# Kernel tuning notes

Measured on AMD Instinct MI355X. Metric: run time of the kernel, lower is better.

The kernel has to match this reference:

```python
import jax, jax.numpy as jnp
import numpy as np

# Straight-through hard softmax (gumbel_softmax with use_gumbel=False, hard=True, dim=1)
def _st_softmax(logits, axis=1):
    soft = jax.nn.softmax(logits, axis=axis)
    hard = jax.nn.one_hot(jnp.argmax(soft, axis=axis), logits.shape[axis], axis=axis, dtype=soft.dtype)
    return soft + jax.lax.stop_gradient(hard - soft)

# gumbel_sigmoid with k=2, hard=True, use_gumbel=False: two straight-through
# one-hot masks selecting the top-1 and top-2 entries along dim=1.
def _st_top2(logits):  # logits: [1, D, S] -> two masks [1, D, S]
    soft = jax.nn.softmax(logits, axis=1)
    D = logits.shape[1]
    _, idx = jax.lax.top_k(jnp.swapaxes(soft, 1, 2), 2)  # [1, S, 2]
    h1 = jnp.swapaxes(jax.nn.one_hot(idx[..., 0], D, dtype=soft.dtype), 1, 2)
    h2 = jnp.swapaxes(jax.nn.one_hot(idx[..., 1], D, dtype=soft.dtype), 1, 2)
    return (soft + jax.lax.stop_gradient(h1 - soft),
            soft + jax.lax.stop_gradient(h2 - soft))

B, CIN, HW, M_IMG, S0 = 8192, 8, 28, 8, 4
S1, S2, M_SC = 3, 2, 2
F_IN, H_IMG, O_IMG = 784, 256, 3  # img_module_arch
H_SC = 12                          # module_arch [2,12,1]

def setup_inputs() -> dict:
    key = jax.random.key(0)
    ks = jax.random.split(key, 16)
    def w(k, shape, fan_in):
        return jax.random.normal(k, shape, jnp.float32) / np.sqrt(fan_in)
    d = {}
    d['x'] = jax.random.normal(ks[0], (B, CIN, HW, HW), jnp.float32)
    # routing embeddings (torch.randn init)
    d['inp_emb0'] = jax.random.normal(ks[1], (1, CIN, S0), jnp.float32)
    d['loc_emb0'] = jax.random.normal(ks[2], (1, M_IMG, S0), jnp.float32)
    d['inp_emb1'] = jax.random.normal(ks[3], (1, S0 * O_IMG, S1), jnp.float32)
    d['loc_emb1'] = jax.random.normal(ks[4], (1, M_SC, S1), jnp.float32)
    d['inp_emb2'] = jax.random.normal(ks[5], (1, S1, S2), jnp.float32)
    d['loc_emb2'] = jax.random.normal(ks[6], (1, M_SC, S2), jnp.float32)
    d['inp_emb3'] = jax.random.normal(ks[7], (1, S2, 1), jnp.float32)
    # img expert MLPs, stacked over M_IMG modules
    d['Wi1'] = w(ks[8], (M_IMG, F_IN, H_IMG), F_IN);  d['bi1'] = jnp.zeros((M_IMG, H_IMG), jnp.float32)
    d['Wi2'] = w(ks[9], (M_IMG, H_IMG, H_IMG), H_IMG); d['bi2'] = jnp.zeros((M_IMG, H_IMG), jnp.float32)
    d['Wi3'] = w(ks[10], (M_IMG, H_IMG, O_IMG), H_IMG); d['bi3'] = jnp.zeros((M_IMG, O_IMG), jnp.float32)
    # scalar expert MLPs [2,12,1], stacked over M_SC modules
    d['Wm1'] = w(ks[11], (M_SC, 2, H_SC), 2);   d['bm1'] = jnp.zeros((M_SC, H_SC), jnp.float32)
    d['Wm2'] = w(ks[12], (M_SC, H_SC, 1), H_SC); d['bm2'] = jnp.zeros((M_SC, 1), jnp.float32)
    return d

def _scalar_level(xv, inp_emb, loc_emb, Wm1, bm1, Wm2, bm2):
    s1, s2 = _st_top2(inp_emb)             # [1, D, S]
    v1 = xv @ s1[0]                        # [B, S]
    v2 = xv @ s2[0]                        # [B, S]
    inp = jnp.stack([v1, v2], axis=-1)     # [B, S, 2]
    h = jax.nn.relu(jnp.einsum('bsi,mij->bsmj', inp, Wm1) + bm1)  # [B,S,M,12]
    o = (jnp.einsum('bsmj,mjo->bsmo', h, Wm2) + bm2)[..., 0]      # [B,S,M]
    s_loc = _st_softmax(loc_emb)[0]        # [M, S]
    return jnp.einsum('bsm,ms->bs', o, s_loc)

def reference(x, inp_emb0, loc_emb0, inp_emb1, loc_emb1, inp_emb2, loc_emb2,
              inp_emb3, Wi1, bi1, Wi2, bi2, Wi3, bi3, Wm1, bm1, Wm2, bm2):
    b = x.shape[0]
    # ---- img level ----
    s_inp = _st_softmax(inp_emb0)[0]                 # [CIN, S0]
    s_loc = _st_softmax(loc_emb0)[0]                 # [M_IMG, S0]
    slot = jnp.einsum('bchw,cs->bshw', x, s_inp)     # channel select per slot
    xf = slot.reshape(b, slot.shape[1], -1)          # [B, S0, 784]
    h = jax.nn.relu(jnp.einsum('bsf,mfk->bsmk', xf, Wi1) + bi1)
    h = jax.nn.relu(jnp.einsum('bsmk,mkj->bsmj', h, Wi2) + bi2)
    o = jnp.einsum('bsmj,mjo->bsmo', h, Wi3) + bi3   # [B, S0, M_IMG, 3]
    y = jnp.einsum('bsmo,ms->bso', o, s_loc)         # weighted sum over modules
    xv = y.reshape(b, -1)                            # [B, S0*3] slot-major cat
    # ---- scalar levels ----
    xv = _scalar_level(xv, inp_emb1, loc_emb1, Wm1, bm1, Wm2, bm2)  # [B, 3]
    xv = _scalar_level(xv, inp_emb2, loc_emb2, Wm1, bm1, Wm2, bm2)  # [B, 2]
    # ---- task output ----
    s1, s2 = _st_top2(inp_emb3)
    v1 = xv @ s1[0]                                  # [B, 1]
    v2 = xv @ s2[0]                                  # [B, 1]
    return jax.nn.sigmoid(jnp.concatenate([v1, v2], axis=1))
```

## Files before the change

### kernel.cpp

```cpp
#include <hip/hip_runtime.h>
#include <hip/hip_bf16.h>
#include <stdint.h>

typedef __attribute__((ext_vector_type(8))) short  bf16x8;
typedef __attribute__((ext_vector_type(4))) float  f32x4;
typedef __attribute__((ext_vector_type(8))) unsigned short u16x8;

__device__ __forceinline__ unsigned short f2bf(float f) {
    union { float f; uint32_t u; } v; v.f = f;
    uint32_t u = v.u;
    uint32_t r = (u + 0x7FFFu + ((u >> 16) & 1u)) >> 16;
    return (unsigned short)r;
}
__device__ __forceinline__ float bf2f(unsigned short h) {
    union { uint32_t u; float f; } v; v.u = ((uint32_t)h) << 16;
    return v.f;
}

#define BATCH 8192
#define CIN   8
#define S0    4
#define FIN   784
#define KP1   800
#define HDIM  256
#define APITCH 40
#define HPITCH 264

#define W1T_OFF 0
#define W1T_BYTES (8u * 256u * 800u * 2u)
#define W2T_OFF (W1T_OFF + W1T_BYTES)
#define W2T_BYTES (8u * 256u * 256u * 2u)
#define YWS_OFF (W2T_OFF + W2T_BYTES)
#define WS_NEED (YWS_OFF + (size_t)BATCH * 12u * 4u)

__device__ __forceinline__ void scalar_tail(const float* xv,
    const float* __restrict__ inp1, const float* __restrict__ loc1,
    const float* __restrict__ inp2, const float* __restrict__ loc2,
    const float* __restrict__ inp3,
    const float* __restrict__ Wm1, const float* __restrict__ bm1,
    const float* __restrict__ Wm2, const float* __restrict__ bm2,
    float* out2)
{
    float xv1[3];
#pragma unroll
    for (int s = 0; s < 3; ++s) {
        int i1 = 0, i2 = 0; float b1v = inp1[s], b2v = -3.0e38f;
        for (int d = 1; d < 12; ++d) {
            float v = inp1[d * 3 + s];
            if (v > b1v)      { b2v = b1v; i2 = i1; b1v = v; i1 = d; }
            else if (v > b2v) { b2v = v; i2 = d; }
        }
        int m = (loc1[3 + s] > loc1[s]) ? 1 : 0;
        float v1 = xv[i1], v2 = xv[i2];
        float o = bm2[m];
#pragma unroll
        for (int j = 0; j < 12; ++j) {
            float h = v1 * Wm1[(m * 2 + 0) * 12 + j] + v2 * Wm1[(m * 2 + 1) * 12 + j] + bm1[m * 12 + j];
            h = fmaxf(h, 0.f);
            o += h * Wm2[m * 12 + j];
        }
        xv1[s] = o;
    }
    float xv2[2];
#pragma unroll
    for (int s = 0; s < 2; ++s) {
        int i1 = 0, i2 = 0; float b1v = inp2[s], b2v = -3.0e38f;
        for (int d = 1; d < 3; ++d) {
            float v = inp2[d * 2 + s];
            if (v > b1v)      { b2v = b1v; i2 = i1; b1v = v; i1 = d; }
            else if (v > b2v) { b2v = v; i2 = d; }
        }
        int m = (loc2[2 + s] > loc2[s]) ? 1 : 0;
        float v1 = xv1[i1], v2 = xv1[i2];
        float o = bm2[m];
#pragma unroll
        for (int j = 0; j < 12; ++j) {
            float h = v1 * Wm1[(m * 2 + 0) * 12 + j] + v2 * Wm1[(m * 2 + 1) * 12 + j] + bm1[m * 12 + j];
            h = fmaxf(h, 0.f);
            o += h * Wm2[m * 12 + j];
        }
        xv2[s] = o;
    }
    int j1 = (inp3[1] > inp3[0]) ? 1 : 0;
    int j2 = 1 - j1;
    out2[0] = 1.f / (1.f + expf(-xv2[j1]));
    out2[1] = 1.f / (1.f + expf(-xv2[j2]));
}

__global__ void prep_weights_kernel(const float* __restrict__ Wi1, const float* __restrict__ Wi2,
                                    unsigned short* __restrict__ W1t, unsigned short* __restrict__ W2t)
{
    __shared__ float tile[32][33];
    int bx = blockIdx.x;
    const float* src; unsigned short* dst; int K, Kpad, N, ktiles, ntiles;
    if (bx < 1600) { src = Wi1; dst = W1t; K = 784; Kpad = 800; N = 256; ktiles = 25; ntiles = 8; }
    else { bx -= 1600; src = Wi2; dst = W2t; K = 256; Kpad = 256; N = 256; ktiles = 8; ntiles = 8; }

    int nt = bx % ntiles;
    int kt = (bx / ntiles) % ktiles;
    int m  = bx / (ntiles * ktiles);
    int k0 = kt * 32, n0 = nt * 32;
    int t = threadIdx.x;
    int r  = t >> 3;
    int c4 = (t & 7) * 4;

    float4 v = make_float4(0.f, 0.f, 0.f, 0.f);
    if (k0 + r < K)
        v = *(const float4*)(src + ((size_t)m * K + (k0 + r)) * N + n0 + c4);
    tile[r][c4 + 0] = v.x; tile[r][c4 + 1] = v.y;
    tile[r][c4 + 2] = v.z; tile[r][c4 + 3] = v.w;
    __syncthreads();

    int nr = r, kc = c4;
    ushort4 ov;
    ov.x = f2bf(tile[kc + 0][nr]);
    ov.y = f2bf(tile[kc + 1][nr]);
    ov.z = f2bf(tile[kc + 2][nr]);
    ov.w = f2bf(tile[kc + 3][nr]);
    *(ushort4*)(dst + ((size_t)m * N + n0 + nr) * Kpad + k0 + kc) = ov;
}

__global__ __launch_bounds__(256, 1) void img_gemm_kernel(
    const float* __restrict__ x,
    const float* __restrict__ inp0, const float* __restrict__ loc0,
    const unsigned short* __restrict__ W1t, const unsigned short* __restrict__ W2t,
    const float* __restrict__ bi1, const float* __restrict__ bi2,
    const float* __restrict__ Wi3, const float* __restrict__ bi3,
    float* __restrict__ yws)
{
    __shared__ __align__(16) unsigned short Abuf[2][64 * APITCH];
    __shared__ __align__(16) unsigned short Hbuf[64 * HPITCH];
    __shared__ float bias1s[256];
    __shared__ float bias2s[256];
    __shared__ float W3s[768];
    __shared__ float b3s[3];

    const int t  = threadIdx.x;
    const int s  = blockIdx.x & 3;
    const int rt = blockIdx.x >> 2;
    const int b0 = rt * 64;

    int cs = 0; { float bv = inp0[s];
        for (int c = 1; c < CIN; ++c) { float v = inp0[c * S0 + s]; if (v > bv) { bv = v; cs = c; } } }
    int ms = 0; { float bv = loc0[s];
        for (int m = 1; m < 8; ++m) { float v = loc0[m * S0 + s]; if (v > bv) { bv = v; ms = m; } } }

    bias1s[t] = bi1[ms * 256 + t];
    bias2s[t] = bi2[ms * 256 + t];
    W3s[t * 3 + 0] = Wi3[((size_t)ms * 256 + t) * 3 + 0];
    W3s[t * 3 + 1] = Wi3[((size_t)ms * 256 + t) * 3 + 1];
    W3s[t * 3 + 2] = Wi3[((size_t)ms * 256 + t) * 3 + 2];
    if (t < 3) b3s[t] = bi3[ms * 3 + t];

    const int w    = t >> 6;
    const int l    = t & 63;
    const int quad = l >> 4;
    const int lr   = l & 15;

    f32x4 acc[4][4];
#pragma unroll
    for (int i = 0; i < 4; ++i)
#pragma unroll
        for (int j = 0; j < 4; ++j) acc[i][j] = (f32x4){0.f, 0.f, 0.f, 0.f};

    const int ar = t >> 2;
    const int ak = (t & 3) * 8;
    const float* xrow = x + ((size_t)(b0 + ar) * CIN + cs) * FIN;

    const unsigned short* b1base = W1t + ((size_t)ms * 256 + w * 64 + lr) * KP1 + quad * 8;

    float4 f0 = make_float4(0,0,0,0), f1 = make_float4(0,0,0,0);
    {
        const float* p = xrow + ak;
        f0 = *(const float4*)(p);
        f1 = *(const float4*)(p + 4);
        bf16x8 av;
        av[0] = (short)f2bf(f0.x); av[1] = (short)f2bf(f0.y);
        av[2] = (short)f2bf(f0.z); av[3] = (short)f2bf(f0.w);
        av[4] = (short)f2bf(f1.x); av[5] = (short)f2bf(f1.y);
        av[6] = (short)f2bf(f1.z); av[7] = (short)f2bf(f1.w);
        *(bf16x8*)&Abuf[0][ar * APITCH + ak] = av;
    }
    {
        const float* p = xrow + 32 + ak;
        f0 = *(const float4*)(p);
        f1 = *(const float4*)(p + 4);
    }
    bf16x8 bcur[4];
#pragma unroll
    for (int nt = 0; nt < 4; ++nt)
        bcur[nt] = *(const bf16x8*)(b1base + nt * 16 * KP1);
    __syncthreads();

    for (int kc = 0; kc < 25; ++kc) {
        bf16x8 bnxt[4];
        {
            const int koff_n = (kc < 24) ? (kc + 1) * 32 : 0;
#pragma unroll
            for (int nt = 0; nt < 4; ++nt)
                bnxt[nt] = *(const bf16x8*)(b1base + nt * 16 * KP1 + koff_n);
        }

        if (kc < 24) {
            bf16x8 av;
            int gk = (kc + 1) * 32 + ak;
            if (gk < FIN) {
                av[0] = (short)f2bf(f0.x); av[1] = (short)f2bf(f0.y);
                av[2] = (short)f2bf(f0.z); av[3] = (short)f2bf(f0.w);
                av[4] = (short)f2bf(f1.x); av[5] = (short)f2bf(f1.y);
                av[6] = (short)f2bf(f1.z); av[7] = (short)f2bf(f1.w);
            } else {
                av = (bf16x8){0,0,0,0,0,0,0,0};
            }
            *(bf16x8*)&Abuf[(kc + 1) & 1][ar * APITCH + ak] = av;
            if (kc < 23) {
                int gk2 = (kc + 2) * 32 + ak;
                if (gk2 < FIN) {
                    const float* p = xrow + gk2;
                    f0 = *(const float4*)(p);
                    f1 = *(const float4*)(p + 4);
                }
            }
        }

        const unsigned short* ab = Abuf[kc & 1];
        bf16x8 afr[4];
#pragma unroll
        for (int mt = 0; mt < 4; ++mt)
            afr[mt] = *(const bf16x8*)&ab[(mt * 16 + lr) * APITCH + quad * 8];
#pragma unroll
        for (int mt = 0; mt < 4; ++mt)
#pragma unroll
            for (int nt = 0; nt < 4; ++nt)
                acc[mt][nt] = __builtin_amdgcn_mfma_f32_16x16x32_bf16(afr[mt], bcur[nt], acc[mt][nt], 0, 0, 0);
#pragma unroll
        for (int nt = 0; nt < 4; ++nt) bcur[nt] = bnxt[nt];
        __syncthreads();
    }

    const unsigned short* b2base = W2t + ((size_t)ms * 256 + w * 64 + lr) * 256 + quad * 8;
#pragma unroll
    for (int nt = 0; nt < 4; ++nt)
        bcur[nt] = *(const bf16x8*)(b2base + nt * 16 * 256);

#pragma unroll
    for (int mt = 0; mt < 4; ++mt)
#pragma unroll
        for (int nt = 0; nt < 4; ++nt) {
            int col = w * 64 + nt * 16 + lr;
            float bb = bias1s[col];
#pragma unroll
            for (int r = 0; r < 4; ++r) {
                int row = mt * 16 + quad * 4 + r;
                float v = acc[mt][nt][r] + bb;
                v = fmaxf(v, 0.f);
                Hbuf[row * HPITCH + col] = f2bf(v);
                acc[mt][nt][r] = 0.f;
            }
        }
    __syncthreads();

#pragma unroll
    for (int kc = 0; kc < 8; ++kc) {
        const int k0 = kc * 32;
        bf16x8 bnxt[4];
        {
            const int k0n = (kc < 7) ? (kc + 1) * 32 : 0;
#pragma unroll
            for (int nt = 0; nt < 4; ++nt)
                bnxt[nt] = *(const bf16x8*)(b2base + nt * 16 * 256 + k0n);
        }
        bf16x8 afr[4];
#pragma unroll
        for (int mt = 0; mt < 4; ++mt)
            afr[mt] = *(const bf16x8*)&Hbuf[(mt * 16 + lr) * HPITCH + k0 + quad * 8];
#pragma unroll
        for (int mt = 0; mt < 4; ++mt)
#pragma unroll
            for (int nt = 0; nt < 4; ++nt)
                acc[mt][nt] = __builtin_amdgcn_mfma_f32_16x16x32_bf16(afr[mt], bcur[nt], acc[mt][nt], 0, 0, 0);
#pragma unroll
        for (int nt = 0; nt < 4; ++nt) bcur[nt] = bnxt[nt];
    }
    __syncthreads();

#pragma unroll
    for (int mt = 0; mt < 4; ++mt)
#pragma unroll
        for (int nt = 0; nt < 4; ++nt) {
            int col = w * 64 + nt * 16 + lr;
            float bb = bias2s[col];
#pragma unroll
            for (int r = 0; r < 4; ++r) {
                int row = mt * 16 + quad * 4 + r;
                float v = acc[mt][nt][r] + bb;
                v = fmaxf(v, 0.f);
                Hbuf[row * HPITCH + col] = f2bf(v);
            }
        }
    __syncthreads();

    if (t < 192) {
        int row = t & 63;
        int o   = t >> 6;
        float a3 = b3s[o];
        for (int j = 0; j < 256; j += 8) {
            u16x8 hv = *(const u16x8*)&Hbuf[row * HPITCH + j];
#pragma unroll
            for (int jj = 0; jj < 8; ++jj)
                a3 += bf2f(hv[jj]) * W3s[(j + jj) * 3 + o];
        }
        yws[(size_t)(b0 + row) * 12 + s * 3 + o] = a3;
    }
}

__global__ void tail_kernel(const float* __restrict__ yws,
                            const float* __restrict__ inp1, const float* __restrict__ loc1,
                            const float* __restrict__ inp2, const float* __restrict__ loc2,
                            const float* __restrict__ inp3,
                            const float* __restrict__ Wm1, const float* __restrict__ bm1,
                            const float* __restrict__ Wm2, const float* __restrict__ bm2,
                            float* __restrict__ out)
{
    int b = blockIdx.x * 256 + threadIdx.x;
    float xv[12];
    const float* p = yws + (size_t)b * 12;
#pragma unroll
    for (int i = 0; i < 12; ++i) xv[i] = p[i];
    float o2[2];
    scalar_tail(xv, inp1, loc1, inp2, loc2, inp3, Wm1, bm1, Wm2, bm2, o2);
    out[(size_t)b * 2 + 0] = o2[0];
    out[(size_t)b * 2 + 1] = o2[1];
}

#define BPITCH 40
__global__ __launch_bounds__(256, 1) void fused_all_kernel(
    const float* __restrict__ x,
    const float* __restrict__ inp0, const float* __restrict__ loc0,
    const float* __restrict__ Wi1, const float* __restrict__ bi1,
    const float* __restrict__ Wi2, const float* __restrict__ bi2,
    const float* __restrict__ Wi3, const float* __restrict__ bi3,
    const float* __restrict__ inp1, const float* __restrict__ loc1,
    const float* __restrict__ inp2, const float* __restrict__ loc2,
    const float* __restrict__ inp3,
    const float* __restrict__ Wm1, const float* __restrict__ bm1,
    const float* __restrict__ Wm2, const float* __restrict__ bm2,
    float* __restrict__ out)
{
    __shared__ __align__(16) unsigned short Abuf[64 * APITCH];
    __shared__ __align__(16) unsigned short Bbuf[256 * BPITCH];
    __shared__ __align__(16) unsigned short Hbuf[64 * HPITCH];
    __shared__ float bias1s[256];
    __shared__ float bias2s[256];
    __shared__ float W3s[768];
    __shared__ float b3s[3];

    const int t  = threadIdx.x;
    const int b0 = blockIdx.x * 64;
    const int w    = t >> 6;
    const int l    = t & 63;
    const int quad = l >> 4;
    const int lr   = l & 15;
    const int ar = t >> 2;
    const int ak = (t & 3) * 8;
    const int wk  = t & 31;
    const int wn0 = (t >> 5) * 32;

    float yreg[4];

#pragma unroll 1
    for (int s = 0; s < 4; ++s) {
        int cs = 0; { float bv = inp0[s];
            for (int c = 1; c < CIN; ++c) { float v = inp0[c * S0 + s]; if (v > bv) { bv = v; cs = c; } } }
        int ms = 0; { float bv = loc0[s];
            for (int m = 1; m < 8; ++m) { float v = loc0[m * S0 + s]; if (v > bv) { bv = v; ms = m; } } }

        __syncthreads();
        bias1s[t] = bi1[ms * 256 + t];
        bias2s[t] = bi2[ms * 256 + t];
        W3s[t * 3 + 0] = Wi3[((size_t)ms * 256 + t) * 3 + 0];
        W3s[t * 3 + 1] = Wi3[((size_t)ms * 256 + t) * 3 + 1];
        W3s[t * 3 + 2] = Wi3[((size_t)ms * 256 + t) * 3 + 2];
        if (t < 3) b3s[t] = bi3[ms * 3 + t];

        f32x4 acc[4][4];
#pragma unroll
        for (int i = 0; i < 4; ++i)
#pragma unroll
            for (int j = 0; j < 4; ++j) acc[i][j] = (f32x4){0.f, 0.f, 0.f, 0.f};

        const float* xbase = x + ((size_t)b0 * CIN + cs) * FIN;
        const float* w1m   = Wi1 + (size_t)ms * FIN * 256;

        for (int kc = 0; kc < 25; ++kc) {
            const int k0 = kc * 32;
            {
                int gk = k0 + ak;
                bf16x8 av;
                if (gk < FIN) {
                    const float* p = xbase + (size_t)ar * (CIN * FIN) + gk;
                    float4 f0 = *(const float4*)(p);
                    float4 f1 = *(const float4*)(p + 4);
                    av[0] = (short)f2bf(f0.x); av[1] = (short)f2bf(f0.y);
                    av[2] = (short)f2bf(f0.z); av[3] = (short)f2bf(f0.w);
                    av[4] = (short)f2bf(f1.x); av[5] = (short)f2bf(f1.y);
                    av[6] = (short)f2bf(f1.z); av[7] = (short)f2bf(f1.w);
                } else {
                    av = (bf16x8){0,0,0,0,0,0,0,0};
                }
                *(bf16x8*)&Abuf[ar * APITCH + ak] = av;
            }
            {
                int gk = k0 + wk;
                if (gk < FIN) {
                    const float* wp = w1m + (size_t)gk * 256 + wn0;
#pragma unroll
                    for (int i = 0; i < 32; i += 4) {
                        float4 f = *(const float4*)(wp + i);
                        Bbuf[(wn0 + i + 0) * BPITCH + wk] = f2bf(f.x);
                        Bbuf[(wn0 + i + 1) * BPITCH + wk] = f2bf(f.y);
                        Bbuf[(wn0 + i + 2) * BPITCH + wk] = f2bf(f.z);
                        Bbuf[(wn0 + i + 3) * BPITCH + wk] = f2bf(f.w);
                    }
                } else {
#pragma unroll
                    for (int i = 0; i < 32; ++i)
                        Bbuf[(wn0 + i) * BPITCH + wk] = 0;
                }
            }
            __syncthreads();

            bf16x8 afr[4], bfr[4];
#pragma unroll
            for (int mt = 0; mt < 4; ++mt)
                afr[mt] = *(const bf16x8*)&Abuf[(mt * 16 + lr) * APITCH + quad * 8];
#pragma unroll
            for (int nt = 0; nt < 4; ++nt)
                bfr[nt] = *(const bf16x8*)&Bbuf[(w * 64 + nt * 16 + lr) * BPITCH + quad * 8];
#pragma unroll
            for (int mt = 0; mt < 4; ++mt)
#pragma unroll
                for (int nt = 0; nt < 4; ++nt)
                    acc[mt][nt] = __builtin_amdgcn_mfma_f32_16x16x32_bf16(afr[mt], bfr[nt], acc[mt][nt], 0, 0, 0);
            __syncthreads();
        }

#pragma unroll
        for (int mt = 0; mt < 4; ++mt)
#pragma unroll
            for (int nt = 0; nt < 4; ++nt) {
                int col = w * 64 + nt * 16 + lr;
                float bb = bias1s[col];
#pragma unroll
                for (int r = 0; r < 4; ++r) {
                    int row = mt * 16 + quad * 4 + r;
                    float v = acc[mt][nt][r] + bb;
                    v = fmaxf(v, 0.f);
                    Hbuf[row * HPITCH + col] = f2bf(v);
                    acc[mt][nt][r] = 0.f;
                }
            }
        __syncthreads();

        const float* w2m = Wi2 + (size_t)ms * 256 * 256;
        for (int kc = 0; kc < 8; ++kc) {
            const int k0 = kc * 32;
            {
                const float* wp = w2m + (size_t)(k0 + wk) * 256 + wn0;
#pragma unroll
                for (int i = 0; i < 32; i += 4) {
                    float4 f = *(const float4*)(wp + i);
                    Bbuf[(wn0 + i + 0) * BPITCH + wk] = f2bf(f.x);
                    Bbuf[(wn0 + i + 1) * BPITCH + wk] = f2bf(f.y);
                    Bbuf[(wn0 + i + 2) * BPITCH + wk] = f2bf(f.z);
                    Bbuf[(wn0 + i + 3) * BPITCH + wk] = f2bf(f.w);
                }
            }
            __syncthreads();

            bf16x8 afr[4], bfr[4];
#pragma unroll
            for (int mt = 0; mt < 4; ++mt)
                afr[mt] = *(const bf16x8*)&Hbuf[(mt * 16 + lr) * HPITCH + k0 + quad * 8];
#pragma unroll
            for (int nt = 0; nt < 4; ++nt)
                bfr[nt] = *(const bf16x8*)&Bbuf[(w * 64 + nt * 16 + lr) * BPITCH + quad * 8];
#pragma unroll
            for (int mt = 0; mt < 4; ++mt)
#pragma unroll
                for (int nt = 0; nt < 4; ++nt)
                    acc[mt][nt] = __builtin_amdgcn_mfma_f32_16x16x32_bf16(afr[mt], bfr[nt], acc[mt][nt], 0, 0, 0);
            __syncthreads();
        }

#pragma unroll
        for (int mt = 0; mt < 4; ++mt)
#pragma unroll
            for (int nt = 0; nt < 4; ++nt) {
                int col = w * 64 + nt * 16 + lr;
                float bb = bias2s[col];
#pragma unroll
                for (int r = 0; r < 4; ++r) {
                    int row = mt * 16 + quad * 4 + r;
                    float v = acc[mt][nt][r] + bb;
                    v = fmaxf(v, 0.f);
                    Hbuf[row * HPITCH + col] = f2bf(v);
                }
            }
        __syncthreads();

        if (t < 192) {
            int row = t & 63;
            int o   = t >> 6;
            float a3 = b3s[o];
            for (int j = 0; j < 256; j += 8) {
                u16x8 hv = *(const u16x8*)&Hbuf[row * HPITCH + j];
#pragma unroll
                for (int jj = 0; jj < 8; ++jj)
                    a3 += bf2f(hv[jj]) * W3s[(j + jj) * 3 + o];
            }
            yreg[s] = a3;
        }
    }

    __syncthreads();
    float* ybuf = (float*)Abuf;
    if (t < 192) {
        int row = t & 63;
        int o   = t >> 6;
#pragma unroll
        for (int s = 0; s < 4; ++s)
            ybuf[row * 12 + s * 3 + o] = yreg[s];
    }
    __syncthreads();
    if (t < 64) {
        float xv[12];
#pragma unroll
        for (int i = 0; i < 12; ++i) xv[i] = ybuf[t * 12 + i];
        float o2[2];
        scalar_tail(xv, inp1, loc1, inp2, loc2, inp3, Wm1, bm1, Wm2, bm2, o2);
        out[(size_t)(b0 + t) * 2 + 0] = o2[0];
        out[(size_t)(b0 + t) * 2 + 1] = o2[1];
    }
}

extern "C" void kernel_launch(void* const* d_in, const int* in_sizes, int n_in,
                              void* d_out, int out_size, void* d_ws, size_t ws_size,
                              hipStream_t stream) {
    if (n_in < 18) return;
    const float* x    = (const float*)d_in[0];
    const float* inp0 = (const float*)d_in[1];
    const float* loc0 = (const float*)d_in[2];
    const float* inp1 = (const float*)d_in[3];
    const float* loc1 = (const float*)d_in[4];
    const float* inp2 = (const float*)d_in[5];
    const float* loc2 = (const float*)d_in[6];
    const float* inp3 = (const float*)d_in[7];
    const float* Wi1  = (const float*)d_in[8];
    const float* bi1  = (const float*)d_in[9];
    const float* Wi2  = (const float*)d_in[10];
    const float* bi2  = (const float*)d_in[11];
    const float* Wi3  = (const float*)d_in[12];
    const float* bi3  = (const float*)d_in[13];
    const float* Wm1  = (const float*)d_in[14];
    const float* bm1  = (const float*)d_in[15];
    const float* Wm2  = (const float*)d_in[16];
    const float* bm2  = (const float*)d_in[17];
    float* out = (float*)d_out;

    if (ws_size >= WS_NEED && d_ws != nullptr) {
        unsigned short* W1t = (unsigned short*)((char*)d_ws + W1T_OFF);
        unsigned short* W2t = (unsigned short*)((char*)d_ws + W2T_OFF);
        float*          yws = (float*)((char*)d_ws + YWS_OFF);

        prep_weights_kernel<<<2112, 256, 0, stream>>>(Wi1, Wi2, W1t, W2t);
        img_gemm_kernel<<<512, 256, 0, stream>>>(x, inp0, loc0, W1t, W2t, bi1, bi2, Wi3, bi3, yws);
        tail_kernel<<<BATCH / 256, 256, 0, stream>>>(yws, inp1, loc1, inp2, loc2, inp3,
                                                     Wm1, bm1, Wm2, bm2, out);
    } else {
        fused_all_kernel<<<BATCH / 64, 256, 0, stream>>>(
            x, inp0, loc0, Wi1, bi1, Wi2, bi2, Wi3, bi3,
            inp1, loc1, inp2, loc2, inp3, Wm1, bm1, Wm2, bm2, out);
    }
}
```

Before: 332.6 us.

## Pre-convert selected input channel to bf16 and load GEMM A-operand directly from global

Adds a prep kernel that selects the routed channel per slot and writes a padded bf16 copy of x into workspace. The image GEMM then loads A fragments straight from global memory into registers, which removes the shared-memory staging buffer and the per-iteration barriers. Both GEMM K-loops are restructured into double-buffered register ping-pong with unroll 1. This costs an extra kernel launch plus a round trip of the converted x (about 52 MB written and read back) through memory. The global fragment loads are 16-byte strided reads with no LDS reuse.

```diff
diff --git a/kernel.cpp b/kernel.cpp
--- a/kernel.cpp
+++ b/kernel.cpp
@@ -31,7 +31,10 @@
 #define W2T_OFF (W1T_OFF + W1T_BYTES)
 #define W2T_BYTES (8u * 256u * 256u * 2u)
 #define YWS_OFF (W2T_OFF + W2T_BYTES)
-#define WS_NEED (YWS_OFF + (size_t)BATCH * 12u * 4u)
+#define YWS_BYTES ((size_t)BATCH * 12u * 4u)
+#define XBF_OFF (YWS_OFF + YWS_BYTES)
+#define XBF_BYTES ((size_t)4 * BATCH * KP1 * 2u)
+#define WS_NEED (XBF_OFF + XBF_BYTES)
 
 __device__ __forceinline__ void scalar_tail(const float* xv,
     const float* __restrict__ inp1, const float* __restrict__ loc1,
@@ -120,15 +123,44 @@
     *(ushort4*)(dst + ((size_t)m * N + n0 + nr) * Kpad + k0 + kc) = ov;
 }
 
+__global__ void prep_x_kernel(const float* __restrict__ x, const float* __restrict__ inp0,
+                              unsigned short* __restrict__ xbf)
+{
+    const int bx = blockIdx.x;
+    const int s  = bx & 3;
+    const int r0 = (bx >> 2) * 32;
+    const int t  = threadIdx.x;
+    const int row = r0 + (t >> 3);
+    const int k8  = (t & 7) * 4;
+
+    int cs = 0; { float bv = inp0[s];
+        for (int c = 1; c < CIN; ++c) { float v = inp0[c * S0 + s]; if (v > bv) { bv = v; cs = c; } } }
+
+    const float* xr = x + ((size_t)row * CIN + cs) * FIN;
+    unsigned short* xo = xbf + ((size_t)s * BATCH + row) * KP1;
+#pragma unroll
+    for (int j = 0; j < 25; ++j) {
+        int k = k8 + j * 32;
+        ushort4 ov;
+        if (k < FIN) {
+            float4 f = *(const float4*)(xr + k);
+            ov.x = f2bf(f.x); ov.y = f2bf(f.y);
+            ov.z = f2bf(f.z); ov.w = f2bf(f.w);
+        } else {
+            ov.x = 0; ov.y = 0; ov.z = 0; ov.w = 0;
+        }
+        *(ushort4*)(xo + k) = ov;
+    }
+}
+
 __global__ __launch_bounds__(256, 1) void img_gemm_kernel(
-    const float* __restrict__ x,
-    const float* __restrict__ inp0, const float* __restrict__ loc0,
+    const unsigned short* __restrict__ xbf,
+    const float* __restrict__ loc0,
     const unsigned short* __restrict__ W1t, const unsigned short* __restrict__ W2t,
     const float* __restrict__ bi1, const float* __restrict__ bi2,
     const float* __restrict__ Wi3, const float* __restrict__ bi3,
     float* __restrict__ yws)
 {
-    __shared__ __align__(16) unsigned short Abuf[2][64 * APITCH];
     __shared__ __align__(16) unsigned short Hbuf[64 * HPITCH];
     __shared__ float bias1s[256];
     __shared__ float bias2s[256];
@@ -140,8 +172,6 @@
     const int rt = blockIdx.x >> 2;
     const int b0 = rt * 64;
 
-    int cs = 0; { float bv = inp0[s];
-        for (int c = 1; c < CIN; ++c) { float v = inp0[c * S0 + s]; if (v > bv) { bv = v; cs = c; } } }
     int ms = 0; { float bv = loc0[s];
         for (int m = 1; m < 8; ++m) { float v = loc0[m * S0 + s]; if (v > bv) { bv = v; ms = m; } } }
 
@@ -151,6 +181,7 @@
     W3s[t * 3 + 1] = Wi3[((size_t)ms * 256 + t) * 3 + 1];
     W3s[t * 3 + 2] = Wi3[((size_t)ms * 256 + t) * 3 + 2];
     if (t < 3) b3s[t] = bi3[ms * 3 + t];
+    __syncthreads();
 
     const int w    = t >> 6;
     const int l    = t & 63;
@@ -163,85 +194,57 @@
 #pragma unroll
         for (int j = 0; j < 4; ++j) acc[i][j] = (f32x4){0.f, 0.f, 0.f, 0.f};
 
-    const int ar = t >> 2;
-    const int ak = (t & 3) * 8;
-    const float* xrow = x + ((size_t)(b0 + ar) * CIN + cs) * FIN;
-
-    const unsigned short* b1base = W1t + ((size_t)ms * 256 + w * 64 + lr) * KP1 + quad * 8;
-
-    float4 f0 = make_float4(0,0,0,0), f1 = make_float4(0,0,0,0);
-    {
-        const float* p = xrow + ak;
-        f0 = *(const float4*)(p);
-        f1 = *(const float4*)(p + 4);
-        bf16x8 av;
-        av[0] = (short)f2bf(f0.x); av[1] = (short)f2bf(f0.y);
-        av[2] = (short)f2bf(f0.z); av[3] = (short)f2bf(f0.w);
-        av[4] = (short)f2bf(f1.x); av[5] = (short)f2bf(f1.y);
-        av[6] = (short)f2bf(f1.z); av[7] = (short)f2bf(f1.w);
-        *(bf16x8*)&Abuf[0][ar * APITCH + ak] = av;
-    }
-    {
-        const float* p = xrow + 32 + ak;
-        f0 = *(const float4*)(p);
-        f1 = *(const float4*)(p + 4);
-    }
-    bf16x8 bcur[4];
+    const unsigned short* ap[4];
+#pragma unroll
+    for (int mt = 0; mt < 4; ++mt)
+        ap[mt] = xbf + ((size_t)s * BATCH + b0 + mt * 16 + lr) * KP1 + quad * 8;
+    const unsigned short* bp[4];
 #pragma unroll
     for (int nt = 0; nt < 4; ++nt)
-        bcur[nt] = *(const bf16x8*)(b1base + nt * 16 * KP1);
-    __syncthreads();
-
-    for (int kc = 0; kc < 25; ++kc) {
-        bf16x8 bnxt[4];
-        {
-            const int koff_n = (kc < 24) ? (kc + 1) * 32 : 0;
+        bp[nt] = W1t + ((size_t)ms * 256 + w * 64 + nt * 16 + lr) * KP1 + quad * 8;
+
+    bf16x8 aA[4], aB[4], bA[4], bB[4];
+#pragma unroll
+    for (int mt = 0; mt < 4; ++mt) aA[mt] = *(const bf16x8*)(ap[mt]);
+#pragma unroll
+    for (int nt = 0; nt < 4; ++nt) bA[nt] = *(const bf16x8*)(bp[nt]);
+
+#pragma unroll 1
+    for (int i = 0; i < 12; ++i) {
+#pragma unroll
+        for (int mt = 0; mt < 4; ++mt) aB[mt] = *(const bf16x8*)(ap[mt] + 32);
+#pragma unroll
+        for (int nt = 0; nt < 4; ++nt) bB[nt] = *(const bf16x8*)(bp[nt] + 32);
+#pragma unroll
+        for (int mt = 0; mt < 4; ++mt)
 #pragma unroll
             for (int nt = 0; nt < 4; ++nt)
-                bnxt[nt] = *(const bf16x8*)(b1base + nt * 16 * KP1 + koff_n);
-        }
-
-        if (kc < 24) {
-            bf16x8 av;
-            int gk = (kc + 1) * 32 + ak;
-            if (gk < FIN) {
-                av[0] = (short)f2bf(f0.x); av[1] = (short)f2bf(f0.y);
-                av[2] = (short)f2bf(f0.z); av[3] = (short)f2bf(f0.w);
-                av[4] = (short)f2bf(f1.x); av[5] = (short)f2bf(f1.y);
-                av[6] = (short)f2bf(f1.z); av[7] = (short)f2bf(f1.w);
-            } else {
-                av = (bf16x8){0,0,0,0,0,0,0,0};
-            }
-            *(bf16x8*)&Abuf[(kc + 1) & 1][ar * APITCH + ak] = av;
-            if (kc < 23) {
-                int gk2 = (kc + 2) * 32 + ak;
-                if (gk2 < FIN) {
-                    const float* p = xrow + gk2;
-                    f0 = *(const float4*)(p);
-                    f1 = *(const float4*)(p + 4);
-                }
-            }
-        }
-
-        const unsigned short* ab = Abuf[kc & 1];
-        bf16x8 afr[4];
-#pragma unroll
-        for (int mt = 0; mt < 4; ++mt)
-            afr[mt] = *(const bf16x8*)&ab[(mt * 16 + lr) * APITCH + quad * 8];
+                acc[mt][nt] = __builtin_amdgcn_mfma_f32_16x16x32_bf16(aA[mt], bA[nt], acc[mt][nt], 0, 0, 0);
+#pragma unroll
+        for (int mt = 0; mt < 4; ++mt) ap[mt] += 64;
+#pragma unroll
+        for (int nt = 0; nt < 4; ++nt) bp[nt] += 64;
+#pragma unroll
+        for (int mt = 0; mt < 4; ++mt) aA[mt] = *(const bf16x8*)(ap[mt]);
+#pragma unroll
+        for (int nt = 0; nt < 4; ++nt) bA[nt] = *(const bf16x8*)(bp[nt]);
 #pragma unroll
         for (int mt = 0; mt < 4; ++mt)
 #pragma unroll
             for (int nt = 0; nt < 4; ++nt)
-                acc[mt][nt] = __builtin_amdgcn_mfma_f32_16x16x32_bf16(afr[mt], bcur[nt], acc[mt][nt], 0, 0, 0);
-#pragma unroll
-        for (int nt = 0; nt < 4; ++nt) bcur[nt] = bnxt[nt];
-        __syncthreads();
-    }
-
-    const unsigned short* b2base = W2t + ((size_t)ms * 256 + w * 64 + lr) * 256 + quad * 8;
+                acc[mt][nt] = __builtin_amdgcn_mfma_f32_16x16x32_bf16(aB[mt], bB[nt], acc[mt][nt], 0, 0, 0);
+    }
+#pragma unroll
+    for (int mt = 0; mt < 4; ++mt)
+#pragma unroll
+        for (int nt = 0; nt < 4; ++nt)
+            acc[mt][nt] = __builtin_amdgcn_mfma_f32_16x16x32_bf16(aA[mt], bA[nt], acc[mt][nt], 0, 0, 0);
+
 #pragma unroll
     for (int nt = 0; nt < 4; ++nt)
-        bcur[nt] = *(const bf16x8*)(b2base + nt * 16 * 256);
+        bp[nt] = W2t + ((size_t)ms * 256 + w * 64 + nt * 16 + lr) * 256 + quad * 8;
+#pragma unroll
+    for (int nt = 0; nt < 4; ++nt) bA[nt] = *(const bf16x8*)(bp[nt]);
 
 #pragma unroll
     for (int mt = 0; mt < 4; ++mt)
@@ -260,27 +263,37 @@
         }
     __syncthreads();
 
-#pragma unroll
-    for (int kc = 0; kc < 8; ++kc) {
-        const int k0 = kc * 32;
-        bf16x8 bnxt[4];
+#pragma unroll 1
+    for (int i = 0; i < 4; ++i) {
+        const int k0 = i * 64;
+#pragma unroll
+        for (int nt = 0; nt < 4; ++nt) bB[nt] = *(const bf16x8*)(bp[nt] + 32);
+        bf16x8 afr[4];
+#pragma unroll
+        for (int mt = 0; mt < 4; ++mt)
+            afr[mt] = *(const bf16x8*)&Hbuf[(mt * 16 + lr) * HPITCH + k0 + quad * 8];
+#pragma unroll
+        for (int mt = 0; mt < 4; ++mt)
+#pragma unroll
+            for (int nt = 0; nt < 4; ++nt)
+                acc[mt][nt] = __builtin_amdgcn_mfma_f32_16x16x32_bf16(afr[mt], bA[nt], acc[mt][nt], 0, 0, 0);
+#pragma unroll
+        for (int nt = 0; nt < 4; ++nt) bp[nt] += 64;
         {
-            const int k0n = (kc < 7) ? (kc + 1) * 32 : 0;
+            const unsigned short* bpn = (i < 3) ? bp[0] : (bp[0] - 256);
 #pragma unroll
             for (int nt = 0; nt < 4; ++nt)
-                bnxt[nt] = *(const bf16x8*)(b2base + nt * 16 * 256 + k0n);
-        }
-        bf16x8 afr[4];
-#pragma unroll
-        for (int mt = 0; mt < 4; ++mt)
-            afr[mt] = *(const bf16x8*)&Hbuf[(mt * 16 + lr) * HPITCH + k0 + quad * 8];
+                bA[nt] = *(const bf16x8*)((i < 3) ? bp[nt] : (bp[nt] - 256));
+            (void)bpn;
+        }
+#pragma unroll
+        for (int mt = 0; mt < 4; ++mt)
+            afr[mt] = *(const bf16x8*)&Hbuf[(mt * 16 + lr) * HPITCH + k0 + 32 + quad * 8];
 #pragma unroll
         for (int mt = 0; mt < 4; ++mt)
 #pragma unroll
             for (int nt = 0; nt < 4; ++nt)
-                acc[mt][nt] = __builtin_amdgcn_mfma_f32_16x16x32_bf16(afr[mt], bcur[nt], acc[mt][nt], 0, 0, 0);
-#pragma unroll
-        for (int nt = 0; nt < 4; ++nt) bcur[nt] = bnxt[nt];
+                acc[mt][nt] = __builtin_amdgcn_mfma_f32_16x16x32_bf16(afr[mt], bB[nt], acc[mt][nt], 0, 0, 0);
     }
     __syncthreads();
 
@@ -572,9 +585,11 @@
         unsigned short* W1t = (unsigned short*)((char*)d_ws + W1T_OFF);
         unsigned short* W2t = (unsigned short*)((char*)d_ws + W2T_OFF);
         float*          yws = (float*)((char*)d_ws + YWS_OFF);
+        unsigned short* xbf = (unsigned short*)((char*)d_ws + XBF_OFF);
 
         prep_weights_kernel<<<2112, 256, 0, stream>>>(Wi1, Wi2, W1t, W2t);
-        img_gemm_kernel<<<512, 256, 0, stream>>>(x, inp0, loc0, W1t, W2t, bi1, bi2, Wi3, bi3, yws);
+        prep_x_kernel<<<(BATCH / 32) * 4, 256, 0, stream>>>(x, inp0, xbf);
+        img_gemm_kernel<<<(BATCH / 64) * 4, 256, 0, stream>>>(xbf, loc0, W1t, W2t, bi1, bi2, Wi3, bi3, yws);
         tail_kernel<<<BATCH / 256, 256, 0, stream>>>(yws, inp1, loc1, inp2, loc2, inp3,
                                                      Wm1, bm1, Wm2, bm2, out);
     } else {
```

After: 352.9 us. 1.06x slower.

## Pre-convert selected input channels to padded bf16 in prep kernel

Applied to the files above, without the earlier changes.

Extends the weight-prep kernel with extra blocks that gather the routed input channel per slot, convert it to bf16 and write it into a K-padded workspace buffer. The GEMM kernel then streams bf16 rows directly into LDS, with no fp32 loads or conversion and no edge checks in its inner loop, and its launch bounds are relaxed to allow more resident blocks. In exchange, an extra write and read of about 52 MB of bf16 activations goes through global memory, along with a larger workspace requirement.

```diff
diff --git a/kernel.cpp b/kernel.cpp
--- a/kernel.cpp
+++ b/kernel.cpp
@@ -31,7 +31,10 @@
 #define W2T_OFF (W1T_OFF + W1T_BYTES)
 #define W2T_BYTES (8u * 256u * 256u * 2u)
 #define YWS_OFF (W2T_OFF + W2T_BYTES)
-#define WS_NEED (YWS_OFF + (size_t)BATCH * 12u * 4u)
+#define YWS_BYTES ((size_t)BATCH * 12u * 4u)
+#define XBF_OFF (YWS_OFF + YWS_BYTES)
+#define XBF_BYTES ((size_t)4 * BATCH * KP1 * 2u)
+#define WS_NEED (XBF_OFF + XBF_BYTES)
 
 __device__ __forceinline__ void scalar_tail(const float* xv,
     const float* __restrict__ inp1, const float* __restrict__ loc1,
@@ -87,42 +90,72 @@
     out2[1] = 1.f / (1.f + expf(-xv2[j2]));
 }
 
-__global__ void prep_weights_kernel(const float* __restrict__ Wi1, const float* __restrict__ Wi2,
-                                    unsigned short* __restrict__ W1t, unsigned short* __restrict__ W2t)
+__global__ void prep_kernel(const float* __restrict__ Wi1, const float* __restrict__ Wi2,
+                            const float* __restrict__ x, const float* __restrict__ inp0,
+                            unsigned short* __restrict__ W1t, unsigned short* __restrict__ W2t,
+                            unsigned short* __restrict__ xbf)
 {
     __shared__ float tile[32][33];
     int bx = blockIdx.x;
-    const float* src; unsigned short* dst; int K, Kpad, N, ktiles, ntiles;
-    if (bx < 1600) { src = Wi1; dst = W1t; K = 784; Kpad = 800; N = 256; ktiles = 25; ntiles = 8; }
-    else { bx -= 1600; src = Wi2; dst = W2t; K = 256; Kpad = 256; N = 256; ktiles = 8; ntiles = 8; }
-
-    int nt = bx % ntiles;
-    int kt = (bx / ntiles) % ktiles;
-    int m  = bx / (ntiles * ktiles);
-    int k0 = kt * 32, n0 = nt * 32;
-    int t = threadIdx.x;
-    int r  = t >> 3;
-    int c4 = (t & 7) * 4;
-
-    float4 v = make_float4(0.f, 0.f, 0.f, 0.f);
-    if (k0 + r < K)
-        v = *(const float4*)(src + ((size_t)m * K + (k0 + r)) * N + n0 + c4);
-    tile[r][c4 + 0] = v.x; tile[r][c4 + 1] = v.y;
-    tile[r][c4 + 2] = v.z; tile[r][c4 + 3] = v.w;
-    __syncthreads();
-
-    int nr = r, kc = c4;
-    ushort4 ov;
-    ov.x = f2bf(tile[kc + 0][nr]);
-    ov.y = f2bf(tile[kc + 1][nr]);
-    ov.z = f2bf(tile[kc + 2][nr]);
-    ov.w = f2bf(tile[kc + 3][nr]);
-    *(ushort4*)(dst + ((size_t)m * N + n0 + nr) * Kpad + k0 + kc) = ov;
-}
-
-__global__ __launch_bounds__(256, 1) void img_gemm_kernel(
-    const float* __restrict__ x,
-    const float* __restrict__ inp0, const float* __restrict__ loc0,
+    const int t = threadIdx.x;
+
+    if (bx < 2112) {
+        const float* src; unsigned short* dst; int K, Kpad, N, ktiles, ntiles;
+        if (bx < 1600) { src = Wi1; dst = W1t; K = 784; Kpad = 800; N = 256; ktiles = 25; ntiles = 8; }
+        else { bx -= 1600; src = Wi2; dst = W2t; K = 256; Kpad = 256; N = 256; ktiles = 8; ntiles = 8; }
+
+        int nt = bx % ntiles;
+        int kt = (bx / ntiles) % ktiles;
+        int m  = bx / (ntiles * ktiles);
+        int k0 = kt * 32, n0 = nt * 32;
+        int r  = t >> 3;
+        int c4 = (t & 7) * 4;
+
+        float4 v = make_float4(0.f, 0.f, 0.f, 0.f);
+        if (k0 + r < K)
+            v = *(const float4*)(src + ((size_t)m * K + (k0 + r)) * N + n0 + c4);
+        tile[r][c4 + 0] = v.x; tile[r][c4 + 1] = v.y;
+        tile[r][c4 + 2] = v.z; tile[r][c4 + 3] = v.w;
+        __syncthreads();
+
+        int nr = r, kc = c4;
+        ushort4 ov;
+        ov.x = f2bf(tile[kc + 0][nr]);
+        ov.y = f2bf(tile[kc + 1][nr]);
+        ov.z = f2bf(tile[kc + 2][nr]);
+        ov.w = f2bf(tile[kc + 3][nr]);
+        *(ushort4*)(dst + ((size_t)m * N + n0 + nr) * Kpad + k0 + kc) = ov;
+    } else {
+        bx -= 2112;
+        const int s  = bx & 3;
+        const int r0 = (bx >> 2) * 32;
+        const int row = r0 + (t >> 3);
+        const int k8  = (t & 7) * 4;
+
+        int cs = 0; { float bv = inp0[s];
+            for (int c = 1; c < CIN; ++c) { float v = inp0[c * S0 + s]; if (v > bv) { bv = v; cs = c; } } }
+
+        const float* xr = x + ((size_t)row * CIN + cs) * FIN;
+        unsigned short* xo = xbf + ((size_t)s * BATCH + row) * KP1;
+#pragma unroll
+        for (int j = 0; j < 25; ++j) {
+            int k = k8 + j * 32;
+            ushort4 ov;
+            if (k < FIN) {
+                float4 f = *(const float4*)(xr + k);
+                ov.x = f2bf(f.x); ov.y = f2bf(f.y);
+                ov.z = f2bf(f.z); ov.w = f2bf(f.w);
+            } else {
+                ov.x = 0; ov.y = 0; ov.z = 0; ov.w = 0;
+            }
+            *(ushort4*)(xo + k) = ov;
+        }
+    }
+}
+
+__global__ __launch_bounds__(256, 3) void img_gemm_kernel(
+    const unsigned short* __restrict__ xbf,
+    const float* __restrict__ loc0,
     const unsigned short* __restrict__ W1t, const unsigned short* __restrict__ W2t,
     const float* __restrict__ bi1, const float* __restrict__ bi2,
     const float* __restrict__ Wi3, const float* __restrict__ bi3,
@@ -140,8 +173,6 @@
     const int rt = blockIdx.x >> 2;
     const int b0 = rt * 64;
 
-    int cs = 0; { float bv = inp0[s];
-        for (int c = 1; c < CIN; ++c) { float v = inp0[c * S0 + s]; if (v > bv) { bv = v; cs = c; } } }
     int ms = 0; { float bv = loc0[s];
         for (int m = 1; m < 8; ++m) { float v = loc0[m * S0 + s]; if (v > bv) { bv = v; ms = m; } } }
 
@@ -165,31 +196,19 @@
 
     const int ar = t >> 2;
     const int ak = (t & 3) * 8;
-    const float* xrow = x + ((size_t)(b0 + ar) * CIN + cs) * FIN;
+    const unsigned short* xrow = xbf + ((size_t)s * BATCH + b0 + ar) * KP1;
+    const int ldsw = ar * APITCH + ak;
 
     const unsigned short* b1base = W1t + ((size_t)ms * 256 + w * 64 + lr) * KP1 + quad * 8;
 
-    float4 f0 = make_float4(0,0,0,0), f1 = make_float4(0,0,0,0);
-    {
-        const float* p = xrow + ak;
-        f0 = *(const float4*)(p);
-        f1 = *(const float4*)(p + 4);
-        bf16x8 av;
-        av[0] = (short)f2bf(f0.x); av[1] = (short)f2bf(f0.y);
-        av[2] = (short)f2bf(f0.z); av[3] = (short)f2bf(f0.w);
-        av[4] = (short)f2bf(f1.x); av[5] = (short)f2bf(f1.y);
-        av[6] = (short)f2bf(f1.z); av[7] = (short)f2bf(f1.w);
-        *(bf16x8*)&Abuf[0][ar * APITCH + ak] = av;
-    }
-    {
-        const float* p = xrow + 32 + ak;
-        f0 = *(const float4*)(p);
-        f1 = *(const float4*)(p + 4);
-    }
+    bf16x8 xa_cur = *(const bf16x8*)(xrow + ak);
+    bf16x8 xa_nxt = *(const bf16x8*)(xrow + 32 + ak);
     bf16x8 bcur[4];
 #pragma unroll
     for (int nt = 0; nt < 4; ++nt)
         bcur[nt] = *(const bf16x8*)(b1base + nt * 16 * KP1);
+    *(bf16x8*)&Abuf[0][ldsw] = xa_cur;
+    xa_cur = xa_nxt;
     __syncthreads();
 
     for (int kc = 0; kc < 25; ++kc) {
@@ -200,27 +219,10 @@
             for (int nt = 0; nt < 4; ++nt)
                 bnxt[nt] = *(const bf16x8*)(b1base + nt * 16 * KP1 + koff_n);
         }
-
         if (kc < 24) {
-            bf16x8 av;
-            int gk = (kc + 1) * 32 + ak;
-            if (gk < FIN) {
-                av[0] = (short)f2bf(f0.x); av[1] = (short)f2bf(f0.y);
-                av[2] = (short)f2bf(f0.z); av[3] = (short)f2bf(f0.w);
-                av[4] = (short)f2bf(f1.x); av[5] = (short)f2bf(f1.y);
-                av[6] = (short)f2bf(f1.z); av[7] = (short)f2bf(f1.w);
-            } else {
-                av = (bf16x8){0,0,0,0,0,0,0,0};
-            }
-            *(bf16x8*)&Abuf[(kc + 1) & 1][ar * APITCH + ak] = av;
-            if (kc < 23) {
-                int gk2 = (kc + 2) * 32 + ak;
-                if (gk2 < FIN) {
-                    const float* p = xrow + gk2;
-                    f0 = *(const float4*)(p);
-                    f1 = *(const float4*)(p + 4);
-                }
-            }
+            *(bf16x8*)&Abuf[(kc + 1) & 1][ldsw] = xa_cur;
+            if (kc < 23)
+                xa_nxt = *(const bf16x8*)(xrow + (kc + 2) * 32 + ak);
         }
 
         const unsigned short* ab = Abuf[kc & 1];
@@ -235,6 +237,7 @@
                 acc[mt][nt] = __builtin_amdgcn_mfma_f32_16x16x32_bf16(afr[mt], bcur[nt], acc[mt][nt], 0, 0, 0);
 #pragma unroll
         for (int nt = 0; nt < 4; ++nt) bcur[nt] = bnxt[nt];
+        xa_cur = xa_nxt;
         __syncthreads();
     }
 
@@ -265,10 +268,10 @@
         const int k0 = kc * 32;
         bf16x8 bnxt[4];
         {
-            const int k0n = (kc < 7) ? (kc + 1) * 32 : 0;
+            const int koff_n = (kc < 7) ? (kc + 1) * 32 : 0;
 #pragma unroll
             for (int nt = 0; nt < 4; ++nt)
-                bnxt[nt] = *(const bf16x8*)(b2base + nt * 16 * 256 + k0n);
+                bnxt[nt] = *(const bf16x8*)(b2base + nt * 16 * 256 + koff_n);
         }
         bf16x8 afr[4];
 #pragma unroll
@@ -572,9 +575,10 @@
         unsigned short* W1t = (unsigned short*)((char*)d_ws + W1T_OFF);
         unsigned short* W2t = (unsigned short*)((char*)d_ws + W2T_OFF);
         float*          yws = (float*)((char*)d_ws + YWS_OFF);
-
-        prep_weights_kernel<<<2112, 256, 0, stream>>>(Wi1, Wi2, W1t, W2t);
-        img_gemm_kernel<<<512, 256, 0, stream>>>(x, inp0, loc0, W1t, W2t, bi1, bi2, Wi3, bi3, yws);
+        unsigned short* xbf = (unsigned short*)((char*)d_ws + XBF_OFF);
+
+        prep_kernel<<<2112 + (BATCH / 32) * 4, 256, 0, stream>>>(Wi1, Wi2, x, inp0, W1t, W2t, xbf);
+        img_gemm_kernel<<<(BATCH / 64) * 4, 256, 0, stream>>>(xbf, loc0, W1t, W2t, bi1, bi2, Wi3, bi3, yws);
         tail_kernel<<<BATCH / 256, 256, 0, stream>>>(yws, inp1, loc1, inp2, loc2, inp3,
                                                      Wm1, bm1, Wm2, bm2, out);
     } else {
```

Measured after the change: 350.7 us. 1.05x slower.

## Widen GEMM1 K-step to 64 and interleave slot blocks for L2 reuse

Applied to the files above, without the earlier changes.

The first-layer GEMM loop now handles 64 K elements per iteration instead of 32, using a wider LDS A tile (pitch 104) and 8 prefetched B fragments. This halves the number of barriers and loop iterations, and the final 32-wide chunk is handled in a peeled tail. Block index decoding is also remapped so that adjacent blocks share a slot and process neighbouring row tiles, which should improve L2 reuse of weights and inputs. The cost is higher register pressure from the doubled fragment buffers and more LDS.

```diff
diff --git a/kernel.cpp b/kernel.cpp
--- a/kernel.cpp
+++ b/kernel.cpp
@@ -24,6 +24,7 @@
 #define KP1   800
 #define HDIM  256
 #define APITCH 40
+#define AP2   104
 #define HPITCH 264
 
 #define W1T_OFF 0
@@ -128,7 +129,7 @@
     const float* __restrict__ Wi3, const float* __restrict__ bi3,
     float* __restrict__ yws)
 {
-    __shared__ __align__(16) unsigned short Abuf[2][64 * APITCH];
+    __shared__ __align__(16) unsigned short Abuf[2][64 * AP2];
     __shared__ __align__(16) unsigned short Hbuf[64 * HPITCH];
     __shared__ float bias1s[256];
     __shared__ float bias2s[256];
@@ -136,8 +137,9 @@
     __shared__ float b3s[3];
 
     const int t  = threadIdx.x;
-    const int s  = blockIdx.x & 3;
-    const int rt = blockIdx.x >> 2;
+    const int bx = blockIdx.x;
+    const int s  = (bx & 7) >> 1;
+    const int rt = ((bx >> 3) << 1) | (bx & 1);
     const int b0 = rt * 64;
 
     int cs = 0; { float bv = inp0[s];
@@ -166,76 +168,104 @@
     const int ar = t >> 2;
     const int ak = (t & 3) * 8;
     const float* xrow = x + ((size_t)(b0 + ar) * CIN + cs) * FIN;
+    const int ldsw = ar * AP2 + ak;
 
     const unsigned short* b1base = W1t + ((size_t)ms * 256 + w * 64 + lr) * KP1 + quad * 8;
 
-    float4 f0 = make_float4(0,0,0,0), f1 = make_float4(0,0,0,0);
+    float4 xf0, xf1, xf2, xf3;
+    xf0 = *(const float4*)(xrow + ak);
+    xf1 = *(const float4*)(xrow + ak + 4);
+    xf2 = *(const float4*)(xrow + ak + 32);
+    xf3 = *(const float4*)(xrow + ak + 36);
     {
-        const float* p = xrow + ak;
-        f0 = *(const float4*)(p);
-        f1 = *(const float4*)(p + 4);
-        bf16x8 av;
-        av[0] = (short)f2bf(f0.x); av[1] = (short)f2bf(f0.y);
-        av[2] = (short)f2bf(f0.z); av[3] = (short)f2bf(f0.w);
-        av[4] = (short)f2bf(f1.x); av[5] = (short)f2bf(f1.y);
-        av[6] = (short)f2bf(f1.z); av[7] = (short)f2bf(f1.w);
-        *(bf16x8*)&Abuf[0][ar * APITCH + ak] = av;
+        bf16x8 v0, v1;
+        v0[0]=(short)f2bf(xf0.x); v0[1]=(short)f2bf(xf0.y); v0[2]=(short)f2bf(xf0.z); v0[3]=(short)f2bf(xf0.w);
+        v0[4]=(short)f2bf(xf1.x); v0[5]=(short)f2bf(xf1.y); v0[6]=(short)f2bf(xf1.z); v0[7]=(short)f2bf(xf1.w);
+        v1[0]=(short)f2bf(xf2.x); v1[1]=(short)f2bf(xf2.y); v1[2]=(short)f2bf(xf2.z); v1[3]=(short)f2bf(xf2.w);
+        v1[4]=(short)f2bf(xf3.x); v1[5]=(short)f2bf(xf3.y); v1[6]=(short)f2bf(xf3.z); v1[7]=(short)f2bf(xf3.w);
+        *(bf16x8*)&Abuf[0][ldsw]      = v0;
+        *(bf16x8*)&Abuf[0][ldsw + 32] = v1;
+    }
+    xf0 = *(const float4*)(xrow + 64 + ak);
+    xf1 = *(const float4*)(xrow + 64 + ak + 4);
+    xf2 = *(const float4*)(xrow + 64 + ak + 32);
+    xf3 = *(const float4*)(xrow + 64 + ak + 36);
+    bf16x8 bcur[8], bnxt[8];
+#pragma unroll
+    for (int nt = 0; nt < 4; ++nt) {
+        bcur[nt]     = *(const bf16x8*)(b1base + nt * 16 * KP1);
+        bcur[nt + 4] = *(const bf16x8*)(b1base + nt * 16 * KP1 + 32);
+    }
+    __syncthreads();
+
+#pragma unroll 1
+    for (int j = 0; j < 12; ++j) {
+        {
+            const int c0 = (j < 11) ? (2 * j + 2) * 32 : 768;
+            const int c1 = (j < 11) ? (2 * j + 3) * 32 : 0;
+#pragma unroll
+            for (int nt = 0; nt < 4; ++nt) {
+                bnxt[nt]     = *(const bf16x8*)(b1base + nt * 16 * KP1 + c0);
+                bnxt[nt + 4] = *(const bf16x8*)(b1base + nt * 16 * KP1 + c1);
+            }
+        }
+        {
+            unsigned short* abn = Abuf[(j + 1) & 1];
+            bf16x8 v0, v1;
+            v0[0]=(short)f2bf(xf0.x); v0[1]=(short)f2bf(xf0.y); v0[2]=(short)f2bf(xf0.z); v0[3]=(short)f2bf(xf0.w);
+            v0[4]=(short)f2bf(xf1.x); v0[5]=(short)f2bf(xf1.y); v0[6]=(short)f2bf(xf1.z); v0[7]=(short)f2bf(xf1.w);
+            v1[0]=(short)f2bf(xf2.x); v1[1]=(short)f2bf(xf2.y); v1[2]=(short)f2bf(xf2.z); v1[3]=(short)f2bf(xf2.w);
+            v1[4]=(short)f2bf(xf3.x); v1[5]=(short)f2bf(xf3.y); v1[6]=(short)f2bf(xf3.z); v1[7]=(short)f2bf(xf3.w);
+            *(bf16x8*)&abn[ldsw]      = v0;
+            *(bf16x8*)&abn[ldsw + 32] = v1;
+        }
+        if (j < 10) {
+            const int base = (j + 2) * 64;
+            xf0 = *(const float4*)(xrow + base + ak);
+            xf1 = *(const float4*)(xrow + base + ak + 4);
+            xf2 = *(const float4*)(xrow + base + ak + 32);
+            xf3 = *(const float4*)(xrow + base + ak + 36);
+        } else if (j == 10) {
+            const int g0 = 768 + ak;
+            xf0 = (g0     < FIN) ? *(const float4*)(xrow + g0)     : make_float4(0.f,0.f,0.f,0.f);
+            xf1 = (g0 + 4 < FIN) ? *(const float4*)(xrow + g0 + 4) : make_float4(0.f,0.f,0.f,0.f);
+            xf2 = make_float4(0.f,0.f,0.f,0.f);
+            xf3 = make_float4(0.f,0.f,0.f,0.f);
+        }
+        {
+            const unsigned short* ab = Abuf[j & 1];
+            bf16x8 afr[4];
+#pragma unroll
+            for (int mt = 0; mt < 4; ++mt)
+                afr[mt] = *(const bf16x8*)&ab[(mt * 16 + lr) * AP2 + quad * 8];
+#pragma unroll
+            for (int mt = 0; mt < 4; ++mt)
+#pragma unroll
+                for (int nt = 0; nt < 4; ++nt)
+                    acc[mt][nt] = __builtin_amdgcn_mfma_f32_16x16x32_bf16(afr[mt], bcur[nt], acc[mt][nt], 0, 0, 0);
+#pragma unroll
+            for (int mt = 0; mt < 4; ++mt)
+                afr[mt] = *(const bf16x8*)&ab[(mt * 16 + lr) * AP2 + 32 + quad * 8];
+#pragma unroll
+            for (int mt = 0; mt < 4; ++mt)
+#pragma unroll
+                for (int nt = 0; nt < 4; ++nt)
+                    acc[mt][nt] = __builtin_amdgcn_mfma_f32_16x16x32_bf16(afr[mt], bcur[nt + 4], acc[mt][nt], 0, 0, 0);
+        }
+#pragma unroll
+        for (int q = 0; q < 8; ++q) bcur[q] = bnxt[q];
+        __syncthreads();
     }
     {
-        const float* p = xrow + 32 + ak;
-        f0 = *(const float4*)(p);
-        f1 = *(const float4*)(p + 4);
-    }
-    bf16x8 bcur[4];
-#pragma unroll
-    for (int nt = 0; nt < 4; ++nt)
-        bcur[nt] = *(const bf16x8*)(b1base + nt * 16 * KP1);
-    __syncthreads();
-
-    for (int kc = 0; kc < 25; ++kc) {
-        bf16x8 bnxt[4];
-        {
-            const int koff_n = (kc < 24) ? (kc + 1) * 32 : 0;
-#pragma unroll
-            for (int nt = 0; nt < 4; ++nt)
-                bnxt[nt] = *(const bf16x8*)(b1base + nt * 16 * KP1 + koff_n);
-        }
-
-        if (kc < 24) {
-            bf16x8 av;
-            int gk = (kc + 1) * 32 + ak;
-            if (gk < FIN) {
-                av[0] = (short)f2bf(f0.x); av[1] = (short)f2bf(f0.y);
-                av[2] = (short)f2bf(f0.z); av[3] = (short)f2bf(f0.w);
-                av[4] = (short)f2bf(f1.x); av[5] = (short)f2bf(f1.y);
-                av[6] = (short)f2bf(f1.z); av[7] = (short)f2bf(f1.w);
-            } else {
-                av = (bf16x8){0,0,0,0,0,0,0,0};
-            }
-            *(bf16x8*)&Abuf[(kc + 1) & 1][ar * APITCH + ak] = av;
-            if (kc < 23) {
-                int gk2 = (kc + 2) * 32 + ak;
-                if (gk2 < FIN) {
-                    const float* p = xrow + gk2;
-                    f0 = *(const float4*)(p);
-                    f1 = *(const float4*)(p + 4);
-                }
-            }
-        }
-
-        const unsigned short* ab = Abuf[kc & 1];
         bf16x8 afr[4];
 #pragma unroll
         for (int mt = 0; mt < 4; ++mt)
-            afr[mt] = *(const bf16x8*)&ab[(mt * 16 + lr) * APITCH + quad * 8];
+            afr[mt] = *(const bf16x8*)&Abuf[0][(mt * 16 + lr) * AP2 + quad * 8];
 #pragma unroll
         for (int mt = 0; mt < 4; ++mt)
 #pragma unroll
             for (int nt = 0; nt < 4; ++nt)
                 acc[mt][nt] = __builtin_amdgcn_mfma_f32_16x16x32_bf16(afr[mt], bcur[nt], acc[mt][nt], 0, 0, 0);
-#pragma unroll
-        for (int nt = 0; nt < 4; ++nt) bcur[nt] = bnxt[nt];
-        __syncthreads();
     }
 
     const unsigned short* b2base = W2t + ((size_t)ms * 256 + w * 64 + lr) * 256 + quad * 8;
@@ -263,12 +293,11 @@
 #pragma unroll
     for (int kc = 0; kc < 8; ++kc) {
         const int k0 = kc * 32;
-        bf16x8 bnxt[4];
         {
-            const int k0n = (kc < 7) ? (kc + 1) * 32 : 0;
+            const int koff_n = (kc < 7) ? (kc + 1) * 32 : 0;
 #pragma unroll
             for (int nt = 0; nt < 4; ++nt)
-                bnxt[nt] = *(const bf16x8*)(b2base + nt * 16 * 256 + k0n);
+                bnxt[nt] = *(const bf16x8*)(b2base + nt * 16 * 256 + koff_n);
         }
         bf16x8 afr[4];
 #pragma unroll
```

New measurement: 323.3 us. 2.8% less time.
